# Kernel tuning notes

Hardware: AMD Instinct MI355X
Metric: run time of the kernel (lower is better)

Reference implementation:

```python
import jax, jax.numpy as jnp
import numpy as np

# Config constants (mirror Qwen3_5TextConfig)
H = 1024        # hidden_size
I = 512         # moe_intermediate_size
IS = 2048       # shared_expert_intermediate_size
E = 16          # num_experts
TOP_K = 4       # num_experts_per_tok
NORM_TOPK = True
B, S = 1, 1024


def setup_inputs() -> dict:
    key = jax.random.key(0)
    ks = jax.random.split(key, 10)
    s = 0.02
    return {
        "hidden_states": jax.random.normal(ks[0], (B, S, H), jnp.float32),
        "w_router": (jax.random.normal(ks[1], (H, E), jnp.float32) * s),
        # stacked expert weights; Linear(H->I) stored as [E, H, I] for einsum
        "w_gate": (jax.random.normal(ks[2], (E, H, I), jnp.float32) * s),
        "w_up": (jax.random.normal(ks[3], (E, H, I), jnp.float32) * s),
        "w_down": (jax.random.normal(ks[4], (E, I, H), jnp.float32) * s),
        # shared expert (dense MLP)
        "ws_gate": (jax.random.normal(ks[5], (H, IS), jnp.float32) * s),
        "ws_up": (jax.random.normal(ks[6], (H, IS), jnp.float32) * s),
        "ws_down": (jax.random.normal(ks[7], (IS, H), jnp.float32) * s),
        "w_shared_gate": (jax.random.normal(ks[8], (H, 1), jnp.float32) * s),
    }


def reference(hidden_states, w_router, w_gate, w_up, w_down,
              ws_gate, ws_up, ws_down, w_shared_gate):
    b, sl, hd = hidden_states.shape
    x = hidden_states.reshape(-1, hd)              # [T, H]
    T = x.shape[0]

    # --- router: softmax in fp32, top-k, optional renormalization ---
    router_logits = x @ w_router                   # [T, E]
    probs = jax.nn.softmax(router_logits.astype(jnp.float32), axis=-1)
    top_w, top_i = jax.lax.top_k(probs, TOP_K)     # [T, K]
    if NORM_TOPK:
        top_w = top_w / top_w.sum(axis=-1, keepdims=True)
    # dense per-token expert weights (zeros off the top-k)
    dense_w = jnp.zeros((T, E), x.dtype).at[jnp.arange(T)[:, None], top_i].set(
        top_w.astype(x.dtype))                     # [T, E]

    # --- expert MLPs (SwiGLU), computed for all experts then masked-combined ---
    g = jnp.einsum('th,ehi->tei', x, w_gate)       # [T, E, I]
    u = jnp.einsum('th,ehi->tei', x, w_up)         # [T, E, I]
    expert_out = jnp.einsum('tei,eih->teh', jax.nn.silu(g) * u, w_down)  # [T, E, H]
    moe_out = jnp.einsum('te,teh->th', dense_w, expert_out)             # [T, H]

    # --- shared expert + sigmoid gate ---
    shared = (jax.nn.silu(x @ ws_gate) * (x @ ws_up)) @ ws_down          # [T, H]
    shared_gate = jax.nn.sigmoid(x @ w_shared_gate)                      # [T, 1]
    out = (moe_out + shared_gate * shared).reshape(b, sl, hd)
    return out, router_logits
```

## Files before the change

kernel.cpp:

```cpp
#include <hip/hip_runtime.h>
#include <hip/hip_bf16.h>

#define T_ 1024
#define H_ 1024
#define I_ 512
#define IS_ 2048
#define E_ 16

typedef __attribute__((ext_vector_type(8))) short short8;
typedef __attribute__((ext_vector_type(4))) float f32x4;

__device__ __forceinline__ unsigned short f2bf(float f) {
  unsigned u = __builtin_bit_cast(unsigned, f);
  unsigned r = (u + 0x7fffu + ((u >> 16) & 1u)) >> 16;
  return (unsigned short)r;
}

__device__ __forceinline__ void gload16(const void* g, void* l) {
  __builtin_amdgcn_global_load_lds(
      (const __attribute__((address_space(1))) unsigned int*)g,
      (__attribute__((address_space(3))) unsigned int*)l, 16, 0, 0);
}

__device__ __forceinline__ void transpose_tile(
    const float* __restrict__ src, unsigned short* __restrict__ dst,
    int C, int dld, long sbs, long dbs, int bx, int by, int bz) {
  __shared__ unsigned short tile[64 * 72];
  const float* s = src + (long)bz * sbs + ((long)by * 64) * C + bx * 64;
  int cgrp = threadIdx.x & 15, rgrp = threadIdx.x >> 4;
  int c = cgrp << 2, r0 = rgrp << 2;
  const float* sp = s + (long)r0 * C + c;
  float4 v0 = *(const float4*)(sp);
  float4 v1 = *(const float4*)(sp + C);
  float4 v2 = *(const float4*)(sp + 2 * C);
  float4 v3 = *(const float4*)(sp + 3 * C);
  ushort4 w;
  w = (ushort4){f2bf(v0.x), f2bf(v1.x), f2bf(v2.x), f2bf(v3.x)};
  *(ushort4*)&tile[(c + 0) * 72 + r0] = w;
  w = (ushort4){f2bf(v0.y), f2bf(v1.y), f2bf(v2.y), f2bf(v3.y)};
  *(ushort4*)&tile[(c + 1) * 72 + r0] = w;
  w = (ushort4){f2bf(v0.z), f2bf(v1.z), f2bf(v2.z), f2bf(v3.z)};
  *(ushort4*)&tile[(c + 2) * 72 + r0] = w;
  w = (ushort4){f2bf(v0.w), f2bf(v1.w), f2bf(v2.w), f2bf(v3.w)};
  *(ushort4*)&tile[(c + 3) * 72 + r0] = w;
  __syncthreads();
  int orr = threadIdx.x >> 2;
  int ks = (threadIdx.x & 3) << 4;
  uint4 o0 = *(const uint4*)&tile[orr * 72 + ks];
  uint4 o1 = *(const uint4*)&tile[orr * 72 + ks + 8];
  unsigned short* d = dst + (long)bz * dbs + (long)(bx * 64 + orr) * dld + by * 64 + ks;
  *(uint4*)d = o0;
  *(uint4*)(d + 8) = o1;
}

__global__ __launch_bounds__(256) void k_pre(
    const float* __restrict__ x, const float* __restrict__ wr,
    const float* __restrict__ wshg,
    const float* __restrict__ wg, const float* __restrict__ wu,
    const float* __restrict__ wd, const float* __restrict__ wsg,
    const float* __restrict__ wsu, const float* __restrict__ wsd,
    unsigned short* __restrict__ xb, float* __restrict__ logits_out,
    int* __restrict__ top_i, float* __restrict__ top_w, float* __restrict__ gate_sig,
    unsigned short* __restrict__ WGUT, unsigned short* __restrict__ WDT,
    unsigned short* __restrict__ WSGUT, unsigned short* __restrict__ WSDT) {
  __shared__ float red[4][17];
  int id = blockIdx.x;
  if (id >= T_) {
    id -= T_;
    if (id < 4096) {
      const float* s = id < 2048 ? wg : wu;
      unsigned short* dd = id < 2048 ? WGUT : WGUT + (size_t)I_ * H_;
      int l = id & 2047;
      int bz = l >> 7, r = l & 127;
      transpose_tile(s, dd, I_, H_, (long)H_ * I_, (long)2 * I_ * H_, r & 7, r >> 3, bz);
    } else if (id < 6144) {
      int l = id - 4096;
      int bz = l >> 7, r = l & 127;
      transpose_tile(wd, WDT, H_, I_, (long)I_ * H_, (long)H_ * I_, r & 15, r >> 4, bz);
    } else if (id < 7168) {
      int l = id - 6144;
      const float* s = l < 512 ? wsg : wsu;
      unsigned short* dd = l < 512 ? WSGUT : WSGUT + (size_t)IS_ * H_;
      l &= 511;
      transpose_tile(s, dd, IS_, H_, 0, 0, l & 31, l >> 5, 0);
    } else {
      int l = id - 7168;
      transpose_tile(wsd, WSDT, H_, IS_, 0, 0, l & 15, l >> 4, 0);
    }
    return;
  }
  int t = id, tid = threadIdx.x;
  int h0 = tid << 2;
  float acc[17];
#pragma unroll
  for (int e = 0; e < 17; e++) acc[e] = 0.f;
  float4 xv = *(const float4*)(x + (long)t * H_ + h0);
  float4 wsh = *(const float4*)(wshg + h0);
  ushort4 xo;
  xo.x = f2bf(xv.x); xo.y = f2bf(xv.y); xo.z = f2bf(xv.z); xo.w = f2bf(xv.w);
  *(ushort4*)(xb + (long)t * H_ + h0) = xo;
  float xs[4] = {xv.x, xv.y, xv.z, xv.w};
  float ws[4] = {wsh.x, wsh.y, wsh.z, wsh.w};
#pragma unroll
  for (int j = 0; j < 4; j++) {
    const float4* w4 = (const float4*)(wr + (long)(h0 + j) * 16);
    float4 w0 = w4[0], w1 = w4[1], w2 = w4[2], w3 = w4[3];
    float xvj = xs[j];
    acc[0] += xvj * w0.x; acc[1] += xvj * w0.y; acc[2] += xvj * w0.z; acc[3] += xvj * w0.w;
    acc[4] += xvj * w1.x; acc[5] += xvj * w1.y; acc[6] += xvj * w1.z; acc[7] += xvj * w1.w;
    acc[8] += xvj * w2.x; acc[9] += xvj * w2.y; acc[10] += xvj * w2.z; acc[11] += xvj * w2.w;
    acc[12] += xvj * w3.x; acc[13] += xvj * w3.y; acc[14] += xvj * w3.z; acc[15] += xvj * w3.w;
    acc[16] += xvj * ws[j];
  }
#pragma unroll
  for (int off = 32; off >= 1; off >>= 1) {
#pragma unroll
    for (int e = 0; e < 17; e++) acc[e] += __shfl_xor(acc[e], off, 64);
  }
  int wid = tid >> 6, lane = tid & 63;
  if (lane == 0) {
#pragma unroll
    for (int e = 0; e < 17; e++) red[wid][e] = acc[e];
  }
  __syncthreads();
  if (tid == 0) {
    float a[17];
#pragma unroll
    for (int e = 0; e < 17; e++)
      a[e] = red[0][e] + red[1][e] + red[2][e] + red[3][e];
    float m = a[0];
#pragma unroll
    for (int e = 1; e < 16; e++) m = fmaxf(m, a[e]);
    float p[16], s = 0.f;
#pragma unroll
    for (int e = 0; e < 16; e++) { p[e] = expf(a[e] - m); s += p[e]; }
    float inv = 1.f / s;
#pragma unroll
    for (int e = 0; e < 16; e++) p[e] *= inv;
    int ti[4]; float tw[4]; float tsum = 0.f;
#pragma unroll
    for (int k = 0; k < 4; k++) {
      float best = -1.f; int bi = 0;
#pragma unroll
      for (int e = 0; e < 16; e++)
        if (p[e] > best) { best = p[e]; bi = e; }
      ti[k] = bi; tw[k] = best; tsum += best; p[bi] = -2.f;
    }
    float rn = 1.f / tsum;
#pragma unroll
    for (int e = 0; e < 16; e++) logits_out[(long)t * 16 + e] = a[e];
#pragma unroll
    for (int k = 0; k < 4; k++) {
      top_i[t * 4 + k] = ti[k];
      top_w[t * 4 + k] = tw[k] * rn;
    }
    gate_sig[t] = 1.f / (1.f + expf(-a[16]));
  }
}

__global__ __launch_bounds__(256) void k_build(
    const int* __restrict__ top_i, int* __restrict__ counts,
    int* __restrict__ offsets, int* __restrict__ perm, int* __restrict__ slot_of) {
  __shared__ int cnt[E_], cur[E_];
  int tid = threadIdx.x;
  if (tid < E_) cnt[tid] = 0;
  __syncthreads();
  for (int i = tid; i < T_ * 4; i += 256)
    atomicAdd(&cnt[top_i[i]], 1);
  __syncthreads();
  if (tid == 0) {
    int run = 0;
    for (int e = 0; e < E_; e++) {
      int c = cnt[e];
      counts[e] = c;
      offsets[e] = run;
      cur[e] = run;
      run += c;
    }
  }
  __syncthreads();
  for (int i = tid; i < T_ * 4; i += 256) {
    int e = top_i[i];
    int pos = atomicAdd(&cur[e], 1);
    perm[pos] = i >> 2;
    slot_of[i] = pos;
  }
}

__global__ __launch_bounds__(256) void k_gemm_gu(
    const unsigned short* __restrict__ XB,
    const unsigned short* __restrict__ WSGUT, const unsigned short* __restrict__ WGUT,
    unsigned short* __restrict__ HSB, unsigned short* __restrict__ HB,
    const int* __restrict__ counts, const int* __restrict__ offsets,
    const int* __restrict__ perm) {
  int z = blockIdx.z;
  int mtile = blockIdx.y * 64;
  int ntile = blockIdx.x * 64;
  int M, row_base, uoff, ldd;
  const unsigned short* B0;
  unsigned short* DST;
  const int* pp;
  if (z == 0) {
    M = T_; row_base = 0; B0 = WSGUT; uoff = IS_;
    DST = HSB; ldd = IS_; pp = nullptr;
  } else {
    if (ntile >= I_) return;
    int e = z - 1;
    M = counts[e];
    if (mtile >= M) return;
    row_base = offsets[e];
    B0 = WGUT + (long)e * 2 * I_ * H_;
    uoff = I_;
    DST = HB; ldd = I_; pp = perm;
  }

  __shared__ unsigned short lds[2][6144];

  int tid = threadIdx.x, wid = tid >> 6, lane = tid & 63;
  int sub = lane >> 2;
  int ksw = ((lane & 3) ^ ((sub >> 1) & 3)) << 3;

  int rm = mtile + wid * 16 + sub;
  if (rm > M - 1) rm = M - 1;
  long arow = pp ? (long)pp[row_base + rm] : (long)(row_base + rm);
  const unsigned short* aptr = XB + arow * H_ + ksw;
  int rbn = ntile + wid * 16 + sub;
  const unsigned short* bgptr = B0 + (long)rbn * H_ + ksw;
  const unsigned short* buptr = B0 + (long)(rbn + uoff) * H_ + ksw;
  int soff = wid * 512;

  int fr = lane & 15, quad = lane >> 4;
  int fslot = (quad ^ ((fr >> 1) & 3)) << 3;
  int wm = (wid >> 1) * 32, wn = (wid & 1) * 32;

  f32x4 acc[2][2][2];
#pragma unroll
  for (int h = 0; h < 2; h++)
#pragma unroll
    for (int i = 0; i < 2; i++)
#pragma unroll
      for (int j = 0; j < 2; j++) acc[h][i][j] = (f32x4){0.f, 0.f, 0.f, 0.f};

  const int NK = H_ / 32;
  gload16(aptr, &lds[0][soff]);
  gload16(bgptr, &lds[0][2048 + soff]);
  gload16(buptr, &lds[0][4096 + soff]);

  for (int kt = 0; kt < NK; kt++) {
    int cur = kt & 1;
    if (kt + 1 < NK) {
      int ko = (kt + 1) * 32;
      gload16(aptr + ko, &lds[cur ^ 1][soff]);
      gload16(bgptr + ko, &lds[cur ^ 1][2048 + soff]);
      gload16(buptr + ko, &lds[cur ^ 1][4096 + soff]);
      asm volatile("s_waitcnt vmcnt(3)" ::: "memory");
    } else {
      asm volatile("s_waitcnt vmcnt(0)" ::: "memory");
    }
    __builtin_amdgcn_s_barrier();
    __builtin_amdgcn_sched_barrier(0);
    const unsigned short* As = &lds[cur][0];
    const unsigned short* Bg = &lds[cur][2048];
    const unsigned short* Bu = &lds[cur][4096];
    short8 af[2], bg[2], bu[2];
#pragma unroll
    for (int i = 0; i < 2; i++)
      af[i] = *(const short8*)(&As[(wm + i * 16 + fr) * 32 + fslot]);
#pragma unroll
    for (int j = 0; j < 2; j++) {
      bg[j] = *(const short8*)(&Bg[(wn + j * 16 + fr) * 32 + fslot]);
      bu[j] = *(const short8*)(&Bu[(wn + j * 16 + fr) * 32 + fslot]);
    }
#pragma unroll
    for (int i = 0; i < 2; i++)
#pragma unroll
      for (int j = 0; j < 2; j++) {
        acc[0][i][j] = __builtin_amdgcn_mfma_f32_16x16x32_bf16(af[i], bg[j], acc[0][i][j], 0, 0, 0);
        acc[1][i][j] = __builtin_amdgcn_mfma_f32_16x16x32_bf16(af[i], bu[j], acc[1][i][j], 0, 0, 0);
      }
    asm volatile("s_waitcnt lgkmcnt(0)" ::: "memory");
    __builtin_amdgcn_sched_barrier(0);
    __builtin_amdgcn_s_barrier();
  }

#pragma unroll
  for (int i = 0; i < 2; i++) {
    int m0 = mtile + wm + i * 16 + quad * 4;
#pragma unroll
    for (int j = 0; j < 2; j++) {
      int col = ntile + wn + j * 16 + fr;
#pragma unroll
      for (int r = 0; r < 4; r++) {
        int m = m0 + r;
        if (m < M) {
          float g = acc[0][i][j][r], u = acc[1][i][j][r];
          DST[(long)(row_base + m) * ldd + col] = f2bf(g / (1.f + expf(-g)) * u);
        }
      }
    }
  }
}

__global__ __launch_bounds__(256) void k_gemm_dn(
    const unsigned short* __restrict__ HSB, const unsigned short* __restrict__ WSDT,
    float* __restrict__ SHOUT,
    const unsigned short* __restrict__ HB, const unsigned short* __restrict__ WDT,
    float* __restrict__ YD,
    const int* __restrict__ counts, const int* __restrict__ offsets) {
  int z = blockIdx.z;
  int mtile = blockIdx.y * 64;
  int ntile = blockIdx.x * 64;
  const unsigned short *A, *B;
  int K, M, rb;
  float* Y;
  if (z == 0) {
    A = HSB; K = IS_; M = T_; rb = 0; B = WSDT; Y = SHOUT;
  } else {
    int e = z - 1;
    M = counts[e];
    if (mtile >= M) return;
    rb = offsets[e];
    A = HB; K = I_; B = WDT + (long)e * H_ * I_; Y = YD;
  }

  __shared__ unsigned short lds[2][4096];

  int tid = threadIdx.x, wid = tid >> 6, lane = tid & 63;
  int sub = lane >> 2;
  int ksw = ((lane & 3) ^ ((sub >> 1) & 3)) << 3;

  int rm = mtile + wid * 16 + sub;
  if (rm > M - 1) rm = M - 1;
  const unsigned short* aptr = A + (long)(rb + rm) * K + ksw;
  int rbn = ntile + wid * 16 + sub;
  const unsigned short* bptr = B + (long)rbn * K + ksw;
  int soff = wid * 512;

  int fr = lane & 15, quad = lane >> 4;
  int fslot = (quad ^ ((fr >> 1) & 3)) << 3;
  int wm = (wid >> 1) * 32, wn = (wid & 1) * 32;

  f32x4 acc[2][2];
#pragma unroll
  for (int i = 0; i < 2; i++)
#pragma unroll
    for (int j = 0; j < 2; j++) acc[i][j] = (f32x4){0.f, 0.f, 0.f, 0.f};

  const int NK = K / 32;
  gload16(aptr, &lds[0][soff]);
  gload16(bptr, &lds[0][2048 + soff]);

  for (int kt = 0; kt < NK; kt++) {
    int cur = kt & 1;
    if (kt + 1 < NK) {
      int ko = (kt + 1) * 32;
      gload16(aptr + ko, &lds[cur ^ 1][soff]);
      gload16(bptr + ko, &lds[cur ^ 1][2048 + soff]);
      asm volatile("s_waitcnt vmcnt(2)" ::: "memory");
    } else {
      asm volatile("s_waitcnt vmcnt(0)" ::: "memory");
    }
    __builtin_amdgcn_s_barrier();
    __builtin_amdgcn_sched_barrier(0);
    const unsigned short* As = &lds[cur][0];
    const unsigned short* Bs = &lds[cur][2048];
    short8 af[2], bf[2];
#pragma unroll
    for (int i = 0; i < 2; i++)
      af[i] = *(const short8*)(&As[(wm + i * 16 + fr) * 32 + fslot]);
#pragma unroll
    for (int j = 0; j < 2; j++)
      bf[j] = *(const short8*)(&Bs[(wn + j * 16 + fr) * 32 + fslot]);
#pragma unroll
    for (int i = 0; i < 2; i++)
#pragma unroll
      for (int j = 0; j < 2; j++)
        acc[i][j] = __builtin_amdgcn_mfma_f32_16x16x32_bf16(af[i], bf[j], acc[i][j], 0, 0, 0);
    asm volatile("s_waitcnt lgkmcnt(0)" ::: "memory");
    __builtin_amdgcn_sched_barrier(0);
    __builtin_amdgcn_s_barrier();
  }

#pragma unroll
  for (int i = 0; i < 2; i++) {
    int m0 = mtile + wm + i * 16 + quad * 4;
#pragma unroll
    for (int j = 0; j < 2; j++) {
      int col = ntile + wn + j * 16 + fr;
#pragma unroll
      for (int r = 0; r < 4; r++) {
        int m = m0 + r;
        if (m < M) Y[(long)(rb + m) * H_ + col] = acc[i][j][r];
      }
    }
  }
}

__global__ __launch_bounds__(256) void k_combine(
    const float* __restrict__ Yd, const float* __restrict__ shout,
    const float* __restrict__ gate_sig, const float* __restrict__ top_w,
    const int* __restrict__ slot_of, float* __restrict__ out) {
  int t = blockIdx.x;
  int c = threadIdx.x << 2;
  float4 sh = *(const float4*)(shout + (long)t * H_ + c);
  float gs = gate_sig[t];
  float4 o;
  o.x = gs * sh.x; o.y = gs * sh.y; o.z = gs * sh.z; o.w = gs * sh.w;
#pragma unroll
  for (int k = 0; k < 4; k++) {
    int s = slot_of[t * 4 + k];
    float w = top_w[t * 4 + k];
    float4 v = *(const float4*)(Yd + (long)s * H_ + c);
    o.x += w * v.x; o.y += w * v.y; o.z += w * v.z; o.w += w * v.w;
  }
  *(float4*)(out + (long)t * H_ + c) = o;
}

extern "C" void kernel_launch(void* const* d_in, const int* in_sizes, int n_in,
                              void* d_out, int out_size, void* d_ws, size_t ws_size,
                              hipStream_t stream) {
  const float* x    = (const float*)d_in[0];
  const float* wrt  = (const float*)d_in[1];
  const float* wg   = (const float*)d_in[2];
  const float* wu   = (const float*)d_in[3];
  const float* wd   = (const float*)d_in[4];
  const float* wsg  = (const float*)d_in[5];
  const float* wsu  = (const float*)d_in[6];
  const float* wsd  = (const float*)d_in[7];
  const float* wshg = (const float*)d_in[8];
  float* out = (float*)d_out;
  float* logits_out = out + (long)T_ * H_;

  char* ws = (char*)d_ws;
  size_t off = 0;
  auto take = [&](size_t bytes) -> void* {
    void* p = ws + off;
    off += (bytes + 255) & ~(size_t)255;
    return p;
  };

  unsigned short* XB    = (unsigned short*)take((size_t)T_ * H_ * 2);
  unsigned short* WGUT  = (unsigned short*)take((size_t)E_ * 2 * I_ * H_ * 2);
  unsigned short* WDT   = (unsigned short*)take((size_t)E_ * H_ * I_ * 2);
  unsigned short* WSGUT = (unsigned short*)take((size_t)2 * IS_ * H_ * 2);
  unsigned short* WSDT  = (unsigned short*)take((size_t)H_ * IS_ * 2);
  float*          YD    = (float*)take((size_t)4096 * H_ * 4);
  unsigned short* HSB   = (unsigned short*)take((size_t)T_ * IS_ * 2);
  float*          SHOUT = (float*)take((size_t)T_ * H_ * 4);
  unsigned short* HB    = (unsigned short*)take((size_t)4096 * I_ * 2);
  int*   counts   = (int*)take(64);
  int*   offsets  = (int*)take(64);
  int*   top_i    = (int*)take((size_t)T_ * 4 * 4);
  float* top_w    = (float*)take((size_t)T_ * 4 * 4);
  int*   perm     = (int*)take((size_t)4096 * 4);
  int*   slot_of  = (int*)take((size_t)4096 * 4);
  float* gate_sig = (float*)take((size_t)T_ * 4);

  k_pre<<<8704, 256, 0, stream>>>(x, wrt, wshg, wg, wu, wd, wsg, wsu, wsd,
                                  XB, logits_out, top_i, top_w, gate_sig,
                                  WGUT, WDT, WSGUT, WSDT);
  k_build<<<1, 256, 0, stream>>>(top_i, counts, offsets, perm, slot_of);

  k_gemm_gu<<<dim3(32, 16, 17), 256, 0, stream>>>(XB, WSGUT, WGUT, HSB, HB,
                                                  counts, offsets, perm);
  k_gemm_dn<<<dim3(16, 16, 17), 256, 0, stream>>>(HSB, WSDT, SHOUT, HB, WDT, YD,
                                                  counts, offsets);
  k_combine<<<T_, 256, 0, stream>>>(YD, SHOUT, gate_sig, top_w, slot_of, out);
}
```

Before: 279.7 us.

## Use compact persistent tile lists and triple-buffered LDS pipeline in grouped GEMMs

k_build now emits explicit tile work lists for the shared and per-expert GEMMs, so the gate/up and down GEMM kernels run a grid-stride loop over only the valid tiles. This replaces the large 3D grids in which most expert blocks exited immediately. The k-loop also moves from double to triple buffering, issuing loads two stages ahead and dropping the trailing barrier. In exchange it adds serial tile-list construction in the single-block build kernel and raises LDS use per block, which may reduce occupancy.

```diff
diff --git a/kernel.cpp b/kernel.cpp
--- a/kernel.cpp
+++ b/kernel.cpp
@@ -160,8 +160,9 @@
 
 __global__ __launch_bounds__(256) void k_build(
     const int* __restrict__ top_i, int* __restrict__ counts,
-    int* __restrict__ offsets, int* __restrict__ perm, int* __restrict__ slot_of) {
-  __shared__ int cnt[E_], cur[E_];
+    int* __restrict__ offsets, int* __restrict__ perm, int* __restrict__ slot_of,
+    int* __restrict__ gu_tiles, int* __restrict__ dn_tiles, int* __restrict__ ntl) {
+  __shared__ int cnt[E_], cur[E_], mt[E_], pg[E_];
   int tid = threadIdx.x;
   if (tid < E_) cnt[tid] = 0;
   __syncthreads();
@@ -169,14 +170,19 @@
     atomicAdd(&cnt[top_i[i]], 1);
   __syncthreads();
   if (tid == 0) {
-    int run = 0;
+    int run = 0, trun = 0;
     for (int e = 0; e < E_; e++) {
       int c = cnt[e];
       counts[e] = c;
       offsets[e] = run;
       cur[e] = run;
       run += c;
-    }
+      mt[e] = (c + 63) >> 6;
+      pg[e] = trun;
+      trun += mt[e];
+    }
+    ntl[0] = 512 + trun * 8;
+    ntl[1] = 256 + trun * 16;
   }
   __syncthreads();
   for (int i = tid; i < T_ * 4; i += 256) {
@@ -185,6 +191,25 @@
     perm[pos] = i >> 2;
     slot_of[i] = pos;
   }
+  for (int i = tid; i < 512; i += 256)
+    gu_tiles[i] = ((i >> 5) << 6) | (i & 31);
+  if (tid < 256)
+    dn_tiles[tid] = ((tid >> 4) << 6) | (tid & 15);
+  int trun = pg[E_ - 1] + mt[E_ - 1];
+  for (int i = tid; i < trun * 8; i += 256) {
+    int m = i >> 3, x = i & 7;
+    int e = 0;
+    while (e < E_ - 1 && m >= pg[e] + mt[e]) e++;
+    int y = m - pg[e];
+    gu_tiles[512 + i] = ((e + 1) << 12) | (y << 6) | x;
+  }
+  for (int i = tid; i < trun * 16; i += 256) {
+    int m = i >> 4, x = i & 15;
+    int e = 0;
+    while (e < E_ - 1 && m >= pg[e] + mt[e]) e++;
+    int y = m - pg[e];
+    dn_tiles[256 + i] = ((e + 1) << 12) | (y << 6) | x;
+  }
 }
 
 __global__ __launch_bounds__(256) void k_gemm_gu(
@@ -192,109 +217,116 @@
     const unsigned short* __restrict__ WSGUT, const unsigned short* __restrict__ WGUT,
     unsigned short* __restrict__ HSB, unsigned short* __restrict__ HB,
     const int* __restrict__ counts, const int* __restrict__ offsets,
-    const int* __restrict__ perm) {
-  int z = blockIdx.z;
-  int mtile = blockIdx.y * 64;
-  int ntile = blockIdx.x * 64;
-  int M, row_base, uoff, ldd;
-  const unsigned short* B0;
-  unsigned short* DST;
-  const int* pp;
-  if (z == 0) {
-    M = T_; row_base = 0; B0 = WSGUT; uoff = IS_;
-    DST = HSB; ldd = IS_; pp = nullptr;
-  } else {
-    if (ntile >= I_) return;
-    int e = z - 1;
-    M = counts[e];
-    if (mtile >= M) return;
-    row_base = offsets[e];
-    B0 = WGUT + (long)e * 2 * I_ * H_;
-    uoff = I_;
-    DST = HB; ldd = I_; pp = perm;
-  }
-
-  __shared__ unsigned short lds[2][6144];
+    const int* __restrict__ perm, const int* __restrict__ gu_tiles,
+    const int* __restrict__ ntl) {
+  __shared__ unsigned short lds[3][6144];
 
   int tid = threadIdx.x, wid = tid >> 6, lane = tid & 63;
   int sub = lane >> 2;
   int ksw = ((lane & 3) ^ ((sub >> 1) & 3)) << 3;
-
-  int rm = mtile + wid * 16 + sub;
-  if (rm > M - 1) rm = M - 1;
-  long arow = pp ? (long)pp[row_base + rm] : (long)(row_base + rm);
-  const unsigned short* aptr = XB + arow * H_ + ksw;
-  int rbn = ntile + wid * 16 + sub;
-  const unsigned short* bgptr = B0 + (long)rbn * H_ + ksw;
-  const unsigned short* buptr = B0 + (long)(rbn + uoff) * H_ + ksw;
   int soff = wid * 512;
-
   int fr = lane & 15, quad = lane >> 4;
   int fslot = (quad ^ ((fr >> 1) & 3)) << 3;
   int wm = (wid >> 1) * 32, wn = (wid & 1) * 32;
 
-  f32x4 acc[2][2][2];
-#pragma unroll
-  for (int h = 0; h < 2; h++)
-#pragma unroll
-    for (int i = 0; i < 2; i++)
-#pragma unroll
-      for (int j = 0; j < 2; j++) acc[h][i][j] = (f32x4){0.f, 0.f, 0.f, 0.f};
-
-  const int NK = H_ / 32;
-  gload16(aptr, &lds[0][soff]);
-  gload16(bgptr, &lds[0][2048 + soff]);
-  gload16(buptr, &lds[0][4096 + soff]);
-
-  for (int kt = 0; kt < NK; kt++) {
-    int cur = kt & 1;
-    if (kt + 1 < NK) {
-      int ko = (kt + 1) * 32;
-      gload16(aptr + ko, &lds[cur ^ 1][soff]);
-      gload16(bgptr + ko, &lds[cur ^ 1][2048 + soff]);
-      gload16(buptr + ko, &lds[cur ^ 1][4096 + soff]);
-      asm volatile("s_waitcnt vmcnt(3)" ::: "memory");
+  int n_tiles = ntl[0];
+  for (int w = blockIdx.x; w < n_tiles; w += gridDim.x) {
+    int twd = gu_tiles[w];
+    int z = twd >> 12;
+    int mtile = ((twd >> 6) & 63) * 64;
+    int ntile = (twd & 63) * 64;
+    int M, row_base, uoff, ldd;
+    const unsigned short* B0;
+    unsigned short* DST;
+    const int* pp;
+    if (z == 0) {
+      M = T_; row_base = 0; B0 = WSGUT; uoff = IS_;
+      DST = HSB; ldd = IS_; pp = nullptr;
     } else {
-      asm volatile("s_waitcnt vmcnt(0)" ::: "memory");
-    }
+      int e = z - 1;
+      M = counts[e];
+      row_base = offsets[e];
+      B0 = WGUT + (long)e * 2 * I_ * H_;
+      uoff = I_;
+      DST = HB; ldd = I_; pp = perm;
+    }
+
+    int rm = mtile + wid * 16 + sub;
+    if (rm > M - 1) rm = M - 1;
+    long arow = pp ? (long)pp[row_base + rm] : (long)(row_base + rm);
+    const unsigned short* aptr = XB + arow * H_ + ksw;
+    int rbn = ntile + wid * 16 + sub;
+    const unsigned short* bgptr = B0 + (long)rbn * H_ + ksw;
+    const unsigned short* buptr = B0 + (long)(rbn + uoff) * H_ + ksw;
+
+    f32x4 acc[2][2][2];
+#pragma unroll
+    for (int h = 0; h < 2; h++)
+#pragma unroll
+      for (int i = 0; i < 2; i++)
+#pragma unroll
+        for (int j = 0; j < 2; j++) acc[h][i][j] = (f32x4){0.f, 0.f, 0.f, 0.f};
+
+    auto STAGE = [&](int slot, int kt) {
+      int ko = kt * 32;
+      unsigned short* base = &lds[slot][0];
+      gload16(aptr + ko, base + soff);
+      gload16(bgptr + ko, base + 2048 + soff);
+      gload16(buptr + ko, base + 4096 + soff);
+    };
+
+    const int NK = H_ / 32;
+    asm volatile("s_waitcnt lgkmcnt(0)" ::: "memory");
     __builtin_amdgcn_s_barrier();
     __builtin_amdgcn_sched_barrier(0);
-    const unsigned short* As = &lds[cur][0];
-    const unsigned short* Bg = &lds[cur][2048];
-    const unsigned short* Bu = &lds[cur][4096];
-    short8 af[2], bg[2], bu[2];
-#pragma unroll
-    for (int i = 0; i < 2; i++)
-      af[i] = *(const short8*)(&As[(wm + i * 16 + fr) * 32 + fslot]);
-#pragma unroll
-    for (int j = 0; j < 2; j++) {
-      bg[j] = *(const short8*)(&Bg[(wn + j * 16 + fr) * 32 + fslot]);
-      bu[j] = *(const short8*)(&Bu[(wn + j * 16 + fr) * 32 + fslot]);
-    }
-#pragma unroll
-    for (int i = 0; i < 2; i++)
+    STAGE(0, 0);
+    STAGE(1, 1);
+    int cur = 0, stg = 2;
+    for (int kt = 0; kt < NK; kt++) {
+      if (kt + 1 < NK) asm volatile("s_waitcnt vmcnt(3)" ::: "memory");
+      else             asm volatile("s_waitcnt vmcnt(0)" ::: "memory");
+      __builtin_amdgcn_s_barrier();
+      __builtin_amdgcn_sched_barrier(0);
+      if (kt + 2 < NK) STAGE(stg, kt + 2);
+      __builtin_amdgcn_sched_barrier(0);
+      const unsigned short* As = &lds[cur][0];
+      const unsigned short* Bg = &lds[cur][2048];
+      const unsigned short* Bu = &lds[cur][4096];
+      short8 af[2], bg[2], bu[2];
+#pragma unroll
+      for (int i = 0; i < 2; i++)
+        af[i] = *(const short8*)(&As[(wm + i * 16 + fr) * 32 + fslot]);
 #pragma unroll
       for (int j = 0; j < 2; j++) {
-        acc[0][i][j] = __builtin_amdgcn_mfma_f32_16x16x32_bf16(af[i], bg[j], acc[0][i][j], 0, 0, 0);
-        acc[1][i][j] = __builtin_amdgcn_mfma_f32_16x16x32_bf16(af[i], bu[j], acc[1][i][j], 0, 0, 0);
+        bg[j] = *(const short8*)(&Bg[(wn + j * 16 + fr) * 32 + fslot]);
+        bu[j] = *(const short8*)(&Bu[(wn + j * 16 + fr) * 32 + fslot]);
       }
-    asm volatile("s_waitcnt lgkmcnt(0)" ::: "memory");
-    __builtin_amdgcn_sched_barrier(0);
-    __builtin_amdgcn_s_barrier();
-  }
-
-#pragma unroll
-  for (int i = 0; i < 2; i++) {
-    int m0 = mtile + wm + i * 16 + quad * 4;
-#pragma unroll
-    for (int j = 0; j < 2; j++) {
-      int col = ntile + wn + j * 16 + fr;
-#pragma unroll
-      for (int r = 0; r < 4; r++) {
-        int m = m0 + r;
-        if (m < M) {
-          float g = acc[0][i][j][r], u = acc[1][i][j][r];
-          DST[(long)(row_base + m) * ldd + col] = f2bf(g / (1.f + expf(-g)) * u);
+#pragma unroll
+      for (int i = 0; i < 2; i++)
+#pragma unroll
+        for (int j = 0; j < 2; j++) {
+          acc[0][i][j] = __builtin_amdgcn_mfma_f32_16x16x32_bf16(af[i], bg[j], acc[0][i][j], 0, 0, 0);
+          acc[1][i][j] = __builtin_amdgcn_mfma_f32_16x16x32_bf16(af[i], bu[j], acc[1][i][j], 0, 0, 0);
+        }
+      asm volatile("s_waitcnt lgkmcnt(0)" ::: "memory");
+      __builtin_amdgcn_sched_barrier(0);
+      cur = (cur == 2) ? 0 : cur + 1;
+      stg = (stg == 2) ? 0 : stg + 1;
+    }
+
+#pragma unroll
+    for (int i = 0; i < 2; i++) {
+      int m0 = mtile + wm + i * 16 + quad * 4;
+#pragma unroll
+      for (int j = 0; j < 2; j++) {
+        int col = ntile + wn + j * 16 + fr;
+#pragma unroll
+        for (int r = 0; r < 4; r++) {
+          int m = m0 + r;
+          if (m < M) {
+            float g = acc[0][i][j][r], u = acc[1][i][j][r];
+            DST[(long)(row_base + m) * ldd + col] = f2bf(g / (1.f + expf(-g)) * u);
+          }
         }
       }
     }
@@ -306,91 +338,100 @@
     float* __restrict__ SHOUT,
     const unsigned short* __restrict__ HB, const unsigned short* __restrict__ WDT,
     float* __restrict__ YD,
-    const int* __restrict__ counts, const int* __restrict__ offsets) {
-  int z = blockIdx.z;
-  int mtile = blockIdx.y * 64;
-  int ntile = blockIdx.x * 64;
-  const unsigned short *A, *B;
-  int K, M, rb;
-  float* Y;
-  if (z == 0) {
-    A = HSB; K = IS_; M = T_; rb = 0; B = WSDT; Y = SHOUT;
-  } else {
-    int e = z - 1;
-    M = counts[e];
-    if (mtile >= M) return;
-    rb = offsets[e];
-    A = HB; K = I_; B = WDT + (long)e * H_ * I_; Y = YD;
-  }
-
-  __shared__ unsigned short lds[2][4096];
+    const int* __restrict__ counts, const int* __restrict__ offsets,
+    const int* __restrict__ dn_tiles, const int* __restrict__ ntl) {
+  __shared__ unsigned short lds[3][4096];
 
   int tid = threadIdx.x, wid = tid >> 6, lane = tid & 63;
   int sub = lane >> 2;
   int ksw = ((lane & 3) ^ ((sub >> 1) & 3)) << 3;
-
-  int rm = mtile + wid * 16 + sub;
-  if (rm > M - 1) rm = M - 1;
-  const unsigned short* aptr = A + (long)(rb + rm) * K + ksw;
-  int rbn = ntile + wid * 16 + sub;
-  const unsigned short* bptr = B + (long)rbn * K + ksw;
   int soff = wid * 512;
-
   int fr = lane & 15, quad = lane >> 4;
   int fslot = (quad ^ ((fr >> 1) & 3)) << 3;
   int wm = (wid >> 1) * 32, wn = (wid & 1) * 32;
 
-  f32x4 acc[2][2];
-#pragma unroll
-  for (int i = 0; i < 2; i++)
-#pragma unroll
-    for (int j = 0; j < 2; j++) acc[i][j] = (f32x4){0.f, 0.f, 0.f, 0.f};
-
-  const int NK = K / 32;
-  gload16(aptr, &lds[0][soff]);
-  gload16(bptr, &lds[0][2048 + soff]);
-
-  for (int kt = 0; kt < NK; kt++) {
-    int cur = kt & 1;
-    if (kt + 1 < NK) {
-      int ko = (kt + 1) * 32;
-      gload16(aptr + ko, &lds[cur ^ 1][soff]);
-      gload16(bptr + ko, &lds[cur ^ 1][2048 + soff]);
-      asm volatile("s_waitcnt vmcnt(2)" ::: "memory");
+  int n_tiles = ntl[1];
+  for (int w = blockIdx.x; w < n_tiles; w += gridDim.x) {
+    int twd = dn_tiles[w];
+    int z = twd >> 12;
+    int mtile = ((twd >> 6) & 63) * 64;
+    int ntile = (twd & 63) * 64;
+    const unsigned short *A, *B;
+    int K, M, rb;
+    float* Y;
+    if (z == 0) {
+      A = HSB; K = IS_; M = T_; rb = 0; B = WSDT; Y = SHOUT;
     } else {
-      asm volatile("s_waitcnt vmcnt(0)" ::: "memory");
-    }
+      int e = z - 1;
+      M = counts[e];
+      rb = offsets[e];
+      A = HB; K = I_; B = WDT + (long)e * H_ * I_; Y = YD;
+    }
+
+    int rm = mtile + wid * 16 + sub;
+    if (rm > M - 1) rm = M - 1;
+    const unsigned short* aptr = A + (long)(rb + rm) * K + ksw;
+    int rbn = ntile + wid * 16 + sub;
+    const unsigned short* bptr = B + (long)rbn * K + ksw;
+
+    f32x4 acc[2][2];
+#pragma unroll
+    for (int i = 0; i < 2; i++)
+#pragma unroll
+      for (int j = 0; j < 2; j++) acc[i][j] = (f32x4){0.f, 0.f, 0.f, 0.f};
+
+    auto STAGE = [&](int slot, int kt) {
+      int ko = kt * 32;
+      unsigned short* base = &lds[slot][0];
+      gload16(aptr + ko, base + soff);
+      gload16(bptr + ko, base + 2048 + soff);
+    };
+
+    const int NK = K / 32;
+    asm volatile("s_waitcnt lgkmcnt(0)" ::: "memory");
     __builtin_amdgcn_s_barrier();
     __builtin_amdgcn_sched_barrier(0);
-    const unsigned short* As = &lds[cur][0];
-    const unsigned short* Bs = &lds[cur][2048];
-    short8 af[2], bf[2];
-#pragma unroll
-    for (int i = 0; i < 2; i++)
-      af[i] = *(const short8*)(&As[(wm + i * 16 + fr) * 32 + fslot]);
-#pragma unroll
-    for (int j = 0; j < 2; j++)
-      bf[j] = *(const short8*)(&Bs[(wn + j * 16 + fr) * 32 + fslot]);
-#pragma unroll
-    for (int i = 0; i < 2; i++)
+    STAGE(0, 0);
+    STAGE(1, 1);
+    int cur = 0, stg = 2;
+    for (int kt = 0; kt < NK; kt++) {
+      if (kt + 1 < NK) asm volatile("s_waitcnt vmcnt(2)" ::: "memory");
+      else             asm volatile("s_waitcnt vmcnt(0)" ::: "memory");
+      __builtin_amdgcn_s_barrier();
+      __builtin_amdgcn_sched_barrier(0);
+      if (kt + 2 < NK) STAGE(stg, kt + 2);
+      __builtin_amdgcn_sched_barrier(0);
+      const unsigned short* As = &lds[cur][0];
+      const unsigned short* Bs = &lds[cur][2048];
+      short8 af[2], bf[2];
+#pragma unroll
+      for (int i = 0; i < 2; i++)
+        af[i] = *(const short8*)(&As[(wm + i * 16 + fr) * 32 + fslot]);
 #pragma unroll
       for (int j = 0; j < 2; j++)
-        acc[i][j] = __builtin_amdgcn_mfma_f32_16x16x32_bf16(af[i], bf[j], acc[i][j], 0, 0, 0);
-    asm volatile("s_waitcnt lgkmcnt(0)" ::: "memory");
-    __builtin_amdgcn_sched_barrier(0);
-    __builtin_amdgcn_s_barrier();
-  }
-
-#pragma unroll
-  for (int i = 0; i < 2; i++) {
-    int m0 = mtile + wm + i * 16 + quad * 4;
-#pragma unroll
-    for (int j = 0; j < 2; j++) {
-      int col = ntile + wn + j * 16 + fr;
-#pragma unroll
-      for (int r = 0; r < 4; r++) {
-        int m = m0 + r;
-        if (m < M) Y[(long)(rb + m) * H_ + col] = acc[i][j][r];
+        bf[j] = *(const short8*)(&Bs[(wn + j * 16 + fr) * 32 + fslot]);
+#pragma unroll
+      for (int i = 0; i < 2; i++)
+#pragma unroll
+        for (int j = 0; j < 2; j++)
+          acc[i][j] = __builtin_amdgcn_mfma_f32_16x16x32_bf16(af[i], bf[j], acc[i][j], 0, 0, 0);
+      asm volatile("s_waitcnt lgkmcnt(0)" ::: "memory");
+      __builtin_amdgcn_sched_barrier(0);
+      cur = (cur == 2) ? 0 : cur + 1;
+      stg = (stg == 2) ? 0 : stg + 1;
+    }
+
+#pragma unroll
+    for (int i = 0; i < 2; i++) {
+      int m0 = mtile + wm + i * 16 + quad * 4;
+#pragma unroll
+      for (int j = 0; j < 2; j++) {
+        int col = ntile + wn + j * 16 + fr;
+#pragma unroll
+        for (int r = 0; r < 4; r++) {
+          int m = m0 + r;
+          if (m < M) Y[(long)(rb + m) * H_ + col] = acc[i][j][r];
+        }
       }
     }
   }
@@ -455,15 +496,19 @@
   int*   perm     = (int*)take((size_t)4096 * 4);
   int*   slot_of  = (int*)take((size_t)4096 * 4);
   float* gate_sig = (float*)take((size_t)T_ * 4);
+  int*   gu_tiles = (int*)take((size_t)2048 * 4);
+  int*   dn_tiles = (int*)take((size_t)2048 * 4);
+  int*   ntl      = (int*)take(64);
 
   k_pre<<<8704, 256, 0, stream>>>(x, wrt, wshg, wg, wu, wd, wsg, wsu, wsd,
                                   XB, logits_out, top_i, top_w, gate_sig,
                                   WGUT, WDT, WSGUT, WSDT);
-  k_build<<<1, 256, 0, stream>>>(top_i, counts, offsets, perm, slot_of);
-
-  k_gemm_gu<<<dim3(32, 16, 17), 256, 0, stream>>>(XB, WSGUT, WGUT, HSB, HB,
-                                                  counts, offsets, perm);
-  k_gemm_dn<<<dim3(16, 16, 17), 256, 0, stream>>>(HSB, WSDT, SHOUT, HB, WDT, YD,
-                                                  counts, offsets);
+  k_build<<<1, 256, 0, stream>>>(top_i, counts, offsets, perm, slot_of,
+                                 gu_tiles, dn_tiles, ntl);
+
+  k_gemm_gu<<<1024, 256, 0, stream>>>(XB, WSGUT, WGUT, HSB, HB,
+                                      counts, offsets, perm, gu_tiles, ntl);
+  k_gemm_dn<<<1280, 256, 0, stream>>>(HSB, WSDT, SHOUT, HB, WDT, YD,
+                                      counts, offsets, dn_tiles, ntl);
   k_combine<<<T_, 256, 0, stream>>>(YD, SHOUT, gate_sig, top_w, slot_of, out);
 }
```

New measurement: 253.1 us. 9.5% less time.
